# Performance work log

Measured on AMD Instinct MI355X. Metric: run time of the kernel, lower is better.

Reference implementation:

```python
import jax, jax.numpy as jnp
import numpy as np

N_QUBITS = 7
N_LAYERS = 2
DIM = 2 ** N_QUBITS  # 128
NORM_FACTOR = 1.0


def _cnot_gather_idx(n):
    # CNOT chain (0,1),(1,2),...,(n-2,n-1) plus wraparound (n-1,0).
    # new_state[x] = old_state[idx[x]]; apply gates in reverse to arange.
    gates = [(i, i + 1) for i in range(n - 1)] + [(n - 1, 0)]
    idx = np.arange(2 ** n)
    for c, t in reversed(gates):
        cbit = 1 << (n - 1 - c)  # pennylane wire 0 = most significant bit
        tbit = 1 << (n - 1 - t)
        idx = np.where((idx & cbit) > 0, idx ^ tbit, idx)
    return jnp.asarray(idx)

CNOT_IDX = _cnot_gather_idx(N_QUBITS)


def silu(x):
    return x * jax.nn.sigmoid(x)


def cayley(A_real, A_imag):
    # Hermitianize then Cayley transform -> unitary, per layer. [L,D,D]
    A = A_real.astype(jnp.complex64) + 1j * A_imag.astype(jnp.complex64)
    A = A + jnp.conj(jnp.swapaxes(A, -1, -2))
    I = jnp.eye(DIM, dtype=A.dtype)
    return jnp.matmul(A - 1j * I, jnp.linalg.inv(A + 1j * I))


def _single_qubit_gate(theta_x, theta_y):
    # combined G = RY(theta_y) @ RX(theta_x) applied to every qubit
    cx, sx = jnp.cos(theta_x / 2), jnp.sin(theta_x / 2)
    cy, sy = jnp.cos(theta_y / 2), jnp.sin(theta_y / 2)
    RX = jnp.stack([jnp.stack([cx + 0j, -1j * sx]), jnp.stack([-1j * sx, cx + 0j])])
    RY = jnp.stack([jnp.stack([cy + 0j, -sy + 0j]), jnp.stack([sy + 0j, cy + 0j])])
    return RY @ RX


def quantum_evolve(psi, coeffs, q_mats):
    # psi: [N, DIM] complex64 normalized state vectors
    N = psi.shape[0]
    for j in range(N_LAYERS):
        psi = psi @ q_mats[j].T  # QubitUnitary: new = U @ old
        G = _single_qubit_gate(coeffs[j, 0], coeffs[j, 1])
        psi = psi.reshape((N,) + (2,) * N_QUBITS)
        for ax in range(1, N_QUBITS + 1):
            psi = jnp.moveaxis(jnp.tensordot(G, psi, axes=((1,), (ax,))), 0, ax)
        psi = psi.reshape(N, DIM)
        psi = psi[:, CNOT_IDX]  # CNOT chain is a fixed basis permutation
    return psi


def setup_inputs() -> dict:
    key = jax.random.key(0)
    ks = jax.random.split(key, 16)
    N, E = 50000, 800000
    in_nf, hid, out_nf = 128, 128, 128
    h = jax.random.normal(ks[0], (N, in_nf), dtype=jnp.float32)
    edge_index = jax.random.randint(ks[1], (2, E), 0, N)
    s = 0.05
    W_e1 = jax.random.normal(ks[2], (2 * in_nf, hid), dtype=jnp.float32) * s
    b_e1 = jnp.zeros((hid,), dtype=jnp.float32)
    W_e2 = jax.random.normal(ks[3], (hid, hid), dtype=jnp.float32) * s
    b_e2 = jnp.zeros((hid,), dtype=jnp.float32)
    W_enc = jax.random.normal(ks[4], (hid + in_nf, DIM), dtype=jnp.float32) * s
    b_enc = jnp.zeros((DIM,), dtype=jnp.float32)
    coeffs = jax.random.normal(ks[5], (N_LAYERS, 2), dtype=jnp.float32) * 0.1
    A_real = jax.random.normal(ks[6], (N_LAYERS, DIM, DIM), dtype=jnp.float32) * 0.01
    A_imag = jax.random.normal(ks[7], (N_LAYERS, DIM, DIM), dtype=jnp.float32) * 0.01
    W_dec = jax.random.normal(ks[8], (DIM, out_nf), dtype=jnp.float32) * s
    b_dec = jnp.zeros((out_nf,), dtype=jnp.float32)
    return {"h": h, "edge_index": edge_index, "W_e1": W_e1, "b_e1": b_e1,
            "W_e2": W_e2, "b_e2": b_e2, "W_enc": W_enc, "b_enc": b_enc,
            "coeffs": coeffs, "A_real": A_real, "A_imag": A_imag,
            "W_dec": W_dec, "b_dec": b_dec}


def reference(h, edge_index, W_e1, b_e1, W_e2, b_e2, W_enc, b_enc,
              coeffs, A_real, A_imag, W_dec, b_dec):
    row, col = edge_index[0], edge_index[1]
    # edge model: mij = MLP([h_src, h_tgt])
    e = jnp.concatenate([h[row], h[col]], axis=1)  # [E, 2*in_nf]
    e = silu(e @ W_e1 + b_e1)
    edge_feat = silu(e @ W_e2 + b_e2)  # [E, hid]
    # node model: scatter-sum aggregation over destination `row`
    agg = jax.ops.segment_sum(edge_feat, row, num_segments=h.shape[0]) / NORM_FACTOR
    q_input = jnp.concatenate([h, agg], axis=1) @ W_enc + b_enc  # [N, DIM]
    norm = jnp.sqrt(jnp.sum(q_input ** 2, axis=1, keepdims=True) + 1e-12)
    psi = (q_input / norm).astype(jnp.complex64)
    q_mats = cayley(A_real, A_imag)  # [L, DIM, DIM] unitary
    psi = quantum_evolve(psi, coeffs, q_mats)
    out = h + (jnp.real(psi) @ W_dec + b_dec)
    return out, edge_feat
```

## Files before the change

### kernel.cpp

```cpp
#include <hip/hip_runtime.h>
#include <math.h>

#define N_NODES 50000
#define N_EDGES 800000
#define NS_ITERS 3

typedef __attribute__((ext_vector_type(8))) short bf16x8;
typedef __attribute__((ext_vector_type(2))) short shortx2;
typedef __attribute__((ext_vector_type(4))) float f32x4;

__device__ __forceinline__ float silu_f(float x) {
    return x / (1.0f + __expf(-x));
}

__device__ __forceinline__ unsigned short f2bf(float x) {
    union { float f; unsigned u; } v; v.f = x;
    unsigned r = v.u + 0x7FFFu + ((v.u >> 16) & 1u);
    return (unsigned short)(r >> 16);
}

__device__ __forceinline__ void atomic_pk_add_bf16(short* addr, shortx2 v) {
    typedef shortx2 __attribute__((address_space(1)))* gp1;
    __builtin_amdgcn_global_atomic_fadd_v2bf16((gp1)(unsigned long long)addr, v);
}

__global__ __launch_bounds__(256) void hbf16_kernel(const float* __restrict__ h,
                                                    short* __restrict__ hbf) {
    int i = blockIdx.x * 256 + threadIdx.x;
    const float4* h4 = (const float4*)h;
    float4 v0 = h4[i * 2], v1 = h4[i * 2 + 1];
    bf16x8 b;
    b[0] = (short)f2bf(v0.x); b[1] = (short)f2bf(v0.y);
    b[2] = (short)f2bf(v0.z); b[3] = (short)f2bf(v0.w);
    b[4] = (short)f2bf(v1.x); b[5] = (short)f2bf(v1.y);
    b[6] = (short)f2bf(v1.z); b[7] = (short)f2bf(v1.w);
    ((bf16x8*)hbf)[i] = b;
}

__global__ __launch_bounds__(1024) void hmat_kernel(const float* __restrict__ A_real,
                                                    const float* __restrict__ A_imag,
                                                    float* __restrict__ H,
                                                    float* __restrict__ X) {
    const int L = blockIdx.x;
    const int t = threadIdx.x;
    const float* ar = A_real + L * 16384;
    const float* ai = A_imag + L * 16384;
    float* hre = H + L * 32768;
    float* him = hre + 16384;
    float* xre = X + L * 32768;
    float* xim = xre + 16384;
    for (int q = 0; q < 16; ++q) {
        int idx = t + 1024 * q;
        int i = idx >> 7, j = idx & 127;
        float hr = ar[idx] + ar[j * 128 + i];
        float hi = ai[idx] - ai[j * 128 + i];
        hre[idx] = hr;
        him[idx] = hi;
        xre[idx] = hr;
        xim[idx] = hi - (i == j ? 1.0f : 0.0f);
    }
}

__global__ __launch_bounds__(512) void ns_t_kernel(const float* __restrict__ H,
                                                   const float* __restrict__ X,
                                                   float* __restrict__ T) {
    const int L = blockIdx.x >> 5;
    const int t = threadIdx.x;
    const int i = (blockIdx.x & 31) * 4 + (t >> 7);
    const int j = t & 127;
    const float* hre = H + L * 32768;
    const float* him = hre + 16384;
    const float* xre = X + L * 32768;
    const float* xim = xre + 16384;
    float accr = 0.f, acci = 0.f;
    #pragma unroll 4
    for (int k = 0; k < 128; ++k) {
        float hr = hre[i * 128 + k], hi = him[i * 128 + k];
        float xr = xre[k * 128 + j], xi = xim[k * 128 + j];
        accr += hr * xr - hi * xi;
        acci += hr * xi + hi * xr;
    }
    T[L * 32768 + i * 128 + j]         = accr - xim[i * 128 + j];
    T[L * 32768 + 16384 + i * 128 + j] = acci + xre[i * 128 + j];
}

__global__ __launch_bounds__(512) void ns_x_kernel(const float* __restrict__ X,
                                                   const float* __restrict__ T,
                                                   float* __restrict__ Xout) {
    const int L = blockIdx.x >> 5;
    const int t = threadIdx.x;
    const int i = (blockIdx.x & 31) * 4 + (t >> 7);
    const int j = t & 127;
    const float* xre = X + L * 32768;
    const float* xim = xre + 16384;
    const float* tre = T + L * 32768;
    const float* tim = tre + 16384;
    float accr = 0.f, acci = 0.f;
    #pragma unroll 4
    for (int k = 0; k < 128; ++k) {
        float xr = xre[i * 128 + k], xi = xim[i * 128 + k];
        float tr = tre[k * 128 + j], ti = tim[k * 128 + j];
        accr += xr * tr - xi * ti;
        acci += xr * ti + xi * tr;
    }
    Xout[L * 32768 + i * 128 + j]         = 2.0f * xre[i * 128 + j] - accr;
    Xout[L * 32768 + 16384 + i * 128 + j] = 2.0f * xim[i * 128 + j] - acci;
}

__global__ __launch_bounds__(1024) void gateperm_kernel(const float* __restrict__ X,
                                                        const float* __restrict__ coeffs,
                                                        float* __restrict__ Y) {
    __shared__ float Mre[128 * 129];
    __shared__ float Mim[128 * 129];
    const int L = blockIdx.x;
    const int t = threadIdx.x;
    const float* xre = X + L * 32768;
    const float* xim = xre + 16384;

    for (int q = 0; q < 16; ++q) {
        int idx = t + 1024 * q;
        int i = idx >> 7, j = idx & 127;
        Mre[i * 129 + j] = (i == j ? 1.0f : 0.0f) + 2.0f * xim[idx];
        Mim[i * 129 + j] = -2.0f * xre[idx];
    }
    __syncthreads();

    const float tx = coeffs[2 * L + 0] * 0.5f;
    const float ty = coeffs[2 * L + 1] * 0.5f;
    const float cx = cosf(tx), sx = sinf(tx), cy = cosf(ty), sy = sinf(ty);
    const float G00r = cx * cy, G00i = sx * sy;
    const float G01r = -cx * sy, G01i = -sx * cy;
    const float G10r = cx * sy, G10i = -sx * cy;
    const float G11r = cx * cy, G11i = -sx * sy;

    for (int st = 0; st < 7; ++st) {
        int b = 1 << st;
        #pragma unroll
        for (int p = 0; p < 8; ++p) {
            int pid = t + 1024 * p;
            int col = pid & 127, ph = pid >> 7;
            int i0 = ((ph >> st) << (st + 1)) | (ph & (b - 1));
            int i1 = i0 | b;
            float v0r = Mre[i0 * 129 + col], v0i = Mim[i0 * 129 + col];
            float v1r = Mre[i1 * 129 + col], v1i = Mim[i1 * 129 + col];
            Mre[i0 * 129 + col] = G00r * v0r - G00i * v0i + G01r * v1r - G01i * v1i;
            Mim[i0 * 129 + col] = G00r * v0i + G00i * v0r + G01r * v1i + G01i * v1r;
            Mre[i1 * 129 + col] = G10r * v0r - G10i * v0i + G11r * v1r - G11i * v1i;
            Mim[i1 * 129 + col] = G10r * v0i + G10i * v0r + G11r * v1i + G11i * v1r;
        }
        __syncthreads();
    }

    const int cs[7] = {6, 5, 4, 3, 2, 1, 0};
    const int ts[7] = {0, 6, 5, 4, 3, 2, 1};
    float* yre = Y + L * 32768;
    float* yim = yre + 16384;
    for (int q = 0; q < 16; ++q) {
        int idx = t + 1024 * q;
        int ii_ = idx >> 7, col = idx & 127;
        int s = ii_;
        #pragma unroll
        for (int m = 0; m < 7; ++m) {
            int cbit = 1 << (6 - cs[m]);
            int tbit = 1 << (6 - ts[m]);
            if (s & cbit) s ^= tbit;
        }
        yre[idx] = Mre[s * 129 + col];
        yim[idx] = Mim[s * 129 + col];
    }
}

__global__ __launch_bounds__(512) void combine1_kernel(const float* __restrict__ Y,
                                                       float* __restrict__ ReM) {
    __shared__ float q1r[16384];
    __shared__ float q1i[16384];
    const int t = threadIdx.x;
    const float* q1re = Y;
    const float* q1im = Y + 16384;
    const float* q2re = Y + 32768;
    const float* q2im = Y + 49152;
    for (int q = 0; q < 32; ++q) {
        q1r[t + 512 * q] = q1re[t + 512 * q];
        q1i[t + 512 * q] = q1im[t + 512 * q];
    }
    __syncthreads();
    int i = blockIdx.x * 4 + (t >> 7);
    int j = t & 127;
    float acc = 0.f;
    for (int k = 0; k < 128; ++k) {
        acc += q2re[i * 128 + k] * q1r[k * 128 + j] - q2im[i * 128 + k] * q1i[k * 128 + j];
    }
    ReM[i * 128 + j] = acc;
}

__global__ __launch_bounds__(512) void combine2_kernel(const float* __restrict__ ReM,
                                                       const float* __restrict__ W_dec,
                                                       short* __restrict__ Dt) {
    __shared__ float ml[16384];
    __shared__ float wl[16384];
    const int t = threadIdx.x;
    for (int q = 0; q < 32; ++q) {
        ml[t + 512 * q] = ReM[t + 512 * q];
        wl[t + 512 * q] = W_dec[t + 512 * q];
    }
    __syncthreads();
    int k = blockIdx.x * 4 + (t >> 7);
    int j = t & 127;
    float acc = 0.f;
    for (int i = 0; i < 128; ++i) {
        acc += ml[i * 128 + k] * wl[i * 128 + j];
    }
    Dt[j * 128 + k] = (short)f2bf(acc);
}

__global__ __launch_bounds__(1024, 4) void edge_kernel(const short* __restrict__ hbf,
                                                       const int* __restrict__ ei,
                                                       const float* __restrict__ W_e1,
                                                       const float* __restrict__ b_e1,
                                                       const float* __restrict__ W_e2,
                                                       const float* __restrict__ b_e2,
                                                       float* __restrict__ ef_out,
                                                       short* __restrict__ agg_bf) {
    __shared__ short w1t[128 * 256];
    __shared__ short w2t[128 * 128];
    __shared__ short c1s[16][1024];

    const int t = threadIdx.x;
    const int lane = t & 63;
    const int w = t >> 6;
    const int l15 = lane & 15;
    const int kg = lane >> 4;

    {
        const float4* w1_4 = (const float4*)W_e1;
        for (int q = 0; q < 8; ++q) {
            int idx4 = t + 1024 * q;
            int k = idx4 >> 5, j4 = idx4 & 31;
            float4 v = w1_4[idx4];
            int j = j4 * 4;
            w1t[(j + 0) * 256 + (k ^ (((j + 0) & 7) << 3))] = (short)f2bf(v.x);
            w1t[(j + 1) * 256 + (k ^ (((j + 1) & 7) << 3))] = (short)f2bf(v.y);
            w1t[(j + 2) * 256 + (k ^ (((j + 2) & 7) << 3))] = (short)f2bf(v.z);
            w1t[(j + 3) * 256 + (k ^ (((j + 3) & 7) << 3))] = (short)f2bf(v.w);
        }
        const float4* w2_4 = (const float4*)W_e2;
        for (int q = 0; q < 4; ++q) {
            int idx4 = t + 1024 * q;
            int k = idx4 >> 5, j4 = idx4 & 31;
            float4 v = w2_4[idx4];
            int j = j4 * 4;
            w2t[(j + 0) * 128 + (k ^ (((j + 0) & 7) << 3))] = (short)f2bf(v.x);
            w2t[(j + 1) * 128 + (k ^ (((j + 1) & 7) << 3))] = (short)f2bf(v.y);
            w2t[(j + 2) * 128 + (k ^ (((j + 2) & 7) << 3))] = (short)f2bf(v.z);
            w2t[(j + 3) * 128 + (k ^ (((j + 3) & 7) << 3))] = (short)f2bf(v.w);
        }
    }
    float b1v[8], b2v[8];
    #pragma unroll
    for (int nf = 0; nf < 8; ++nf) {
        b1v[nf] = b_e1[nf * 16 + l15];
        b2v[nf] = b_e2[nf * 16 + l15];
    }
    __syncthreads();

    const bf16x8* hb8 = (const bf16x8*)hbf;
    short* myc1 = &c1s[w][0];
    const int NW = gridDim.x * 16;
    const int wvid = blockIdx.x * 16 + w;
    const int nt = N_EDGES / 16;

    int tile = wvid;
    int ri = 0, ci = 0;
    if (tile < nt) {
        ri = ei[tile * 16 + l15];
        ci = ei[N_EDGES + tile * 16 + l15];
    }

    for (; tile < nt; ) {
        const int e0 = tile * 16;
        bf16x8 a1[8];
        #pragma unroll
        for (int s = 0; s < 4; ++s) a1[s] = hb8[(size_t)ri * 16 + s * 4 + kg];
        #pragma unroll
        for (int s = 0; s < 4; ++s) a1[4 + s] = hb8[(size_t)ci * 16 + s * 4 + kg];

        const int tn = tile + NW;
        int ri2 = 0, ci2 = 0;
        if (tn < nt) {
            ri2 = ei[tn * 16 + l15];
            ci2 = ei[N_EDGES + tn * 16 + l15];
        }

        f32x4 acc[8];
        #pragma unroll
        for (int nf = 0; nf < 8; ++nf) acc[nf] = (f32x4){0.f, 0.f, 0.f, 0.f};
        #pragma unroll
        for (int s = 0; s < 8; ++s) {
            const int k0 = s * 32 + kg * 8;
            #pragma unroll
            for (int nf = 0; nf < 8; ++nf) {
                int brow = nf * 16 + l15;
                bf16x8 b = *(const bf16x8*)&w1t[brow * 256 + (k0 ^ ((brow & 7) << 3))];
                acc[nf] = __builtin_amdgcn_mfma_f32_16x16x32_bf16(a1[s], b, acc[nf], 0, 0, 0);
            }
        }

        f32x4 acc2[8];
        #pragma unroll
        for (int nf = 0; nf < 8; ++nf) acc2[nf] = (f32x4){0.f, 0.f, 0.f, 0.f};
        #pragma unroll
        for (int half = 0; half < 2; ++half) {
            #pragma unroll
            for (int nfh = 0; nfh < 4; ++nfh) {
                int nf = half * 4 + nfh;
                #pragma unroll
                for (int r = 0; r < 4; ++r) {
                    int row = kg * 4 + r;
                    int c = nfh * 16 + l15;
                    myc1[row * 64 + (c ^ ((row & 7) << 3))] =
                        (short)f2bf(silu_f(acc[nf][r] + b1v[nf]));
                }
            }
            #pragma unroll
            for (int s2l = 0; s2l < 2; ++s2l) {
                int k0h = s2l * 32 + kg * 8;
                bf16x8 a2 = *(const bf16x8*)&myc1[l15 * 64 + (k0h ^ ((l15 & 7) << 3))];
                int k0g = half * 64 + k0h;
                #pragma unroll
                for (int nf = 0; nf < 8; ++nf) {
                    int brow = nf * 16 + l15;
                    bf16x8 b = *(const bf16x8*)&w2t[brow * 128 + (k0g ^ ((brow & 7) << 3))];
                    acc2[nf] = __builtin_amdgcn_mfma_f32_16x16x32_bf16(a2, b, acc2[nf], 0, 0, 0);
                }
            }
        }

        int rw[4];
        #pragma unroll
        for (int r = 0; r < 4; ++r) rw[r] = __shfl(ri, kg * 4 + r);
        #pragma unroll
        for (int r = 0; r < 4; ++r) {
            int erow = kg * 4 + r;
            float* efp = ef_out + (size_t)(e0 + erow) * 128;
            short* agp = agg_bf + (size_t)rw[r] * 128;
            #pragma unroll
            for (int nf = 0; nf < 8; ++nf) {
                int col = nf * 16 + l15;
                float v = silu_f(acc2[nf][r] + b2v[nf]);
                __builtin_nontemporal_store(v, efp + col);
                float vn = __shfl_xor(v, 1);
                if ((l15 & 1) == 0) {
                    shortx2 pk;
                    pk.x = (short)f2bf(v);
                    pk.y = (short)f2bf(vn);
                    atomic_pk_add_bf16(agp + col, pk);
                }
            }
        }

        tile = tn; ri = ri2; ci = ci2;
    }
}

__global__ __launch_bounds__(512, 4) void encode_kernel(const short* __restrict__ hbf,
                                                        const short* __restrict__ agg_bf,
                                                        const float* __restrict__ W_enc,
                                                        const float* __restrict__ b_enc,
                                                        short* __restrict__ v_bf) {
    __shared__ short wet[128 * 256];

    const int t = threadIdx.x;
    const int lane = t & 63;
    const int w = t >> 6;
    const int l15 = lane & 15;
    const int kg = lane >> 4;

    {
        const float4* we4 = (const float4*)W_enc;
        for (int q = 0; q < 16; ++q) {
            int idx4 = t + 512 * q;
            int k = idx4 >> 5, j4 = idx4 & 31;
            float4 v = we4[idx4];
            int j = j4 * 4;
            wet[(j + 0) * 256 + (k ^ (((j + 0) & 7) << 3))] = (short)f2bf(v.x);
            wet[(j + 1) * 256 + (k ^ (((j + 1) & 7) << 3))] = (short)f2bf(v.y);
            wet[(j + 2) * 256 + (k ^ (((j + 2) & 7) << 3))] = (short)f2bf(v.z);
            wet[(j + 3) * 256 + (k ^ (((j + 3) & 7) << 3))] = (short)f2bf(v.w);
        }
    }
    float bj[8];
    #pragma unroll
    for (int nf = 0; nf < 8; ++nf) bj[nf] = b_enc[nf * 16 + l15];
    __syncthreads();

    const bf16x8* hb8 = (const bf16x8*)hbf;
    const bf16x8* ab8 = (const bf16x8*)agg_bf;
    const int NW = gridDim.x * 8;
    const int nt = N_NODES / 16;

    for (int tile = blockIdx.x * 8 + w; tile < nt; tile += NW) {
        const int node = tile * 16 + l15;
        bf16x8 a[8];
        #pragma unroll
        for (int s = 0; s < 4; ++s) a[s] = hb8[(size_t)node * 16 + s * 4 + kg];
        #pragma unroll
        for (int s = 0; s < 4; ++s) a[4 + s] = ab8[(size_t)node * 16 + s * 4 + kg];

        f32x4 acc[8];
        #pragma unroll
        for (int nf = 0; nf < 8; ++nf) acc[nf] = (f32x4){0.f, 0.f, 0.f, 0.f};
        #pragma unroll
        for (int s = 0; s < 8; ++s) {
            const int k0 = s * 32 + kg * 8;
            #pragma unroll
            for (int nf = 0; nf < 8; ++nf) {
                int brow = nf * 16 + l15;
                bf16x8 b = *(const bf16x8*)&wet[brow * 256 + (k0 ^ ((brow & 7) << 3))];
                acc[nf] = __builtin_amdgcn_mfma_f32_16x16x32_bf16(a[s], b, acc[nf], 0, 0, 0);
            }
        }

        float nr[4] = {0.f, 0.f, 0.f, 0.f};
        #pragma unroll
        for (int nf = 0; nf < 8; ++nf) {
            #pragma unroll
            for (int r = 0; r < 4; ++r) {
                acc[nf][r] += bj[nf];
                nr[r] += acc[nf][r] * acc[nf][r];
            }
        }
        #pragma unroll
        for (int r = 0; r < 4; ++r) {
            nr[r] += __shfl_xor(nr[r], 1);
            nr[r] += __shfl_xor(nr[r], 2);
            nr[r] += __shfl_xor(nr[r], 4);
            nr[r] += __shfl_xor(nr[r], 8);
            nr[r] = 1.0f / sqrtf(nr[r] + 1e-12f);
        }
        #pragma unroll
        for (int r = 0; r < 4; ++r) {
            size_t rowb = (size_t)(tile * 16 + kg * 4 + r) * 128;
            #pragma unroll
            for (int nf = 0; nf < 8; ++nf) {
                v_bf[rowb + nf * 16 + l15] = (short)f2bf(acc[nf][r] * nr[r]);
            }
        }
    }
}

__global__ __launch_bounds__(512, 4) void decode_kernel(const short* __restrict__ v_bf,
                                                        const float* __restrict__ h,
                                                        const short* __restrict__ Dt_bf,
                                                        const float* __restrict__ b_dec,
                                                        float* __restrict__ out) {
    __shared__ short dt[128 * 128];

    const int t = threadIdx.x;
    const int lane = t & 63;
    const int w = t >> 6;
    const int l15 = lane & 15;
    const int kg = lane >> 4;

    {
        const int4* s4 = (const int4*)Dt_bf;
        for (int q = 0; q < 4; ++q) {
            int idx4 = t + 512 * q;
            int j = idx4 >> 4, c = idx4 & 15;
            int k0 = c * 8;
            int4 v = s4[idx4];
            *(int4*)&dt[j * 128 + (k0 ^ ((j & 7) << 3))] = v;
        }
    }
    float bj[8];
    #pragma unroll
    for (int nf = 0; nf < 8; ++nf) bj[nf] = b_dec[nf * 16 + l15];
    __syncthreads();

    const bf16x8* vb8 = (const bf16x8*)v_bf;
    const int NW = gridDim.x * 8;
    const int nt = N_NODES / 16;

    for (int tile = blockIdx.x * 8 + w; tile < nt; tile += NW) {
        const int node = tile * 16 + l15;
        bf16x8 a[4];
        #pragma unroll
        for (int s = 0; s < 4; ++s) a[s] = vb8[(size_t)node * 16 + s * 4 + kg];

        f32x4 acc[8];
        #pragma unroll
        for (int nf = 0; nf < 8; ++nf) acc[nf] = (f32x4){0.f, 0.f, 0.f, 0.f};
        #pragma unroll
        for (int s = 0; s < 4; ++s) {
            const int k0 = s * 32 + kg * 8;
            #pragma unroll
            for (int nf = 0; nf < 8; ++nf) {
                int brow = nf * 16 + l15;
                bf16x8 b = *(const bf16x8*)&dt[brow * 128 + (k0 ^ ((brow & 7) << 3))];
                acc[nf] = __builtin_amdgcn_mfma_f32_16x16x32_bf16(a[s], b, acc[nf], 0, 0, 0);
            }
        }
        #pragma unroll
        for (int r = 0; r < 4; ++r) {
            size_t rowb = (size_t)(tile * 16 + kg * 4 + r) * 128;
            #pragma unroll
            for (int nf = 0; nf < 8; ++nf) {
                int col = nf * 16 + l15;
                out[rowb + col] = h[rowb + col] + acc[nf][r] + bj[nf];
            }
        }
    }
}

extern "C" void kernel_launch(void* const* d_in, const int* in_sizes, int n_in,
                              void* d_out, int out_size, void* d_ws, size_t ws_size,
                              hipStream_t stream) {
    const float* h      = (const float*)d_in[0];
    const int*   ei     = (const int*)d_in[1];
    const float* W_e1   = (const float*)d_in[2];
    const float* b_e1   = (const float*)d_in[3];
    const float* W_e2   = (const float*)d_in[4];
    const float* b_e2   = (const float*)d_in[5];
    const float* W_enc  = (const float*)d_in[6];
    const float* b_enc  = (const float*)d_in[7];
    const float* coeffs = (const float*)d_in[8];
    const float* A_real = (const float*)d_in[9];
    const float* A_imag = (const float*)d_in[10];
    const float* W_dec  = (const float*)d_in[11];
    const float* b_dec  = (const float*)d_in[12];

    float* out    = (float*)d_out;
    float* ef_out = out + (size_t)N_NODES * 128;

    short* agg_bf = (short*)d_ws;
    short* v_bf   = agg_bf + (size_t)N_NODES * 128;
    short* h_bf   = v_bf + (size_t)N_NODES * 128;
    float* small  = (float*)(h_bf + (size_t)N_NODES * 128);
    float* Ybuf   = small;
    float* ReM    = Ybuf + 65536;
    float* Hbuf   = ReM + 16384;
    float* Xa     = Hbuf + 65536;
    float* Xb     = Xa + 65536;
    float* Tbuf   = Xb + 65536;
    short* Dt_bf  = (short*)(Tbuf + 65536);

    hipMemsetAsync(agg_bf, 0, (size_t)N_NODES * 128 * sizeof(short), stream);

    hbf16_kernel<<<3125, 256, 0, stream>>>(h, h_bf);

    hmat_kernel<<<2, 1024, 0, stream>>>(A_real, A_imag, Hbuf, Xa);
    float* xc = Xa;
    float* xn = Xb;
    for (int it = 0; it < NS_ITERS; ++it) {
        ns_t_kernel<<<64, 512, 0, stream>>>(Hbuf, xc, Tbuf);
        ns_x_kernel<<<64, 512, 0, stream>>>(xc, Tbuf, xn);
        float* tmp = xc; xc = xn; xn = tmp;
    }
    gateperm_kernel<<<2, 1024, 0, stream>>>(xc, coeffs, Ybuf);
    combine1_kernel<<<32, 512, 0, stream>>>(Ybuf, ReM);
    combine2_kernel<<<32, 512, 0, stream>>>(ReM, W_dec, Dt_bf);

    edge_kernel<<<256, 1024, 0, stream>>>(h_bf, ei, W_e1, b_e1, W_e2, b_e2, ef_out, agg_bf);

    encode_kernel<<<256, 512, 0, stream>>>(h_bf, agg_bf, W_enc, b_enc, v_bf);

    decode_kernel<<<256, 512, 0, stream>>>(v_bf, h, Dt_bf, b_dec, out);
}
```

Baseline: 623.3 us.

## Fuse encode and decode into one node kernel, prefetch edge gathers, cut NS iterations

Encode and decode are merged into a single node kernel. The normalized quantum state now passes through per-wave LDS into the decode MFMA instead of round-tripping through a bf16 global buffer. The edge kernel software-pipelines the next tile's h-row gathers behind the current tile's MFMAs, at the cost of more registers. The Newton-Schulz iteration count for the matrix inverse drops from 3 to 2, which lowers accuracy of the Cayley unitary and could break correctness tolerance.

```diff
diff --git a/kernel.cpp b/kernel.cpp
--- a/kernel.cpp
+++ b/kernel.cpp
@@ -3,7 +3,7 @@
 
 #define N_NODES 50000
 #define N_EDGES 800000
-#define NS_ITERS 3
+#define NS_ITERS 2
 
 typedef __attribute__((ext_vector_type(8))) short bf16x8;
 typedef __attribute__((ext_vector_type(2))) short shortx2;
@@ -266,29 +266,31 @@
     const bf16x8* hb8 = (const bf16x8*)hbf;
     short* myc1 = &c1s[w][0];
     const int NW = gridDim.x * 16;
-    const int wvid = blockIdx.x * 16 + w;
     const int nt = N_EDGES / 16;
 
-    int tile = wvid;
-    int ri = 0, ci = 0;
-    if (tile < nt) {
-        ri = ei[tile * 16 + l15];
-        ci = ei[N_EDGES + tile * 16 + l15];
-    }
-
-    for (; tile < nt; ) {
+    int tile = blockIdx.x * 16 + w;
+    if (tile >= nt) return;
+    int ri = ei[tile * 16 + l15];
+    int ci = ei[N_EDGES + tile * 16 + l15];
+    bf16x8 a1[8];
+    #pragma unroll
+    for (int s = 0; s < 4; ++s) a1[s] = hb8[(size_t)ri * 16 + s * 4 + kg];
+    #pragma unroll
+    for (int s = 0; s < 4; ++s) a1[4 + s] = hb8[(size_t)ci * 16 + s * 4 + kg];
+    int tn = tile + NW;
+    bool more = (tn < nt);
+    int rin = 0, cin = 0;
+    if (more) {
+        rin = ei[tn * 16 + l15];
+        cin = ei[N_EDGES + tn * 16 + l15];
+    }
+
+    for (;;) {
         const int e0 = tile * 16;
-        bf16x8 a1[8];
-        #pragma unroll
-        for (int s = 0; s < 4; ++s) a1[s] = hb8[(size_t)ri * 16 + s * 4 + kg];
-        #pragma unroll
-        for (int s = 0; s < 4; ++s) a1[4 + s] = hb8[(size_t)ci * 16 + s * 4 + kg];
-
-        const int tn = tile + NW;
-        int ri2 = 0, ci2 = 0;
-        if (tn < nt) {
-            ri2 = ei[tn * 16 + l15];
-            ci2 = ei[N_EDGES + tn * 16 + l15];
+        bf16x8 a1n[8];
+        if (more) {
+            #pragma unroll
+            for (int s = 0; s < 4; ++s) a1n[s] = hb8[(size_t)rin * 16 + s * 4 + kg];
         }
 
         f32x4 acc[8];
@@ -303,6 +305,11 @@
                 bf16x8 b = *(const bf16x8*)&w1t[brow * 256 + (k0 ^ ((brow & 7) << 3))];
                 acc[nf] = __builtin_amdgcn_mfma_f32_16x16x32_bf16(a1[s], b, acc[nf], 0, 0, 0);
             }
+        }
+
+        if (more) {
+            #pragma unroll
+            for (int s = 0; s < 4; ++s) a1n[4 + s] = hb8[(size_t)cin * 16 + s * 4 + kg];
         }
 
         f32x4 acc2[8];
@@ -358,16 +365,31 @@
             }
         }
 
-        tile = tn; ri = ri2; ci = ci2;
-    }
-}
-
-__global__ __launch_bounds__(512, 4) void encode_kernel(const short* __restrict__ hbf,
-                                                        const short* __restrict__ agg_bf,
-                                                        const float* __restrict__ W_enc,
-                                                        const float* __restrict__ b_enc,
-                                                        short* __restrict__ v_bf) {
+        if (!more) break;
+        tile = tn;
+        ri = rin;
+        #pragma unroll
+        for (int s = 0; s < 8; ++s) a1[s] = a1n[s];
+        tn = tile + NW;
+        more = (tn < nt);
+        if (more) {
+            rin = ei[tn * 16 + l15];
+            cin = ei[N_EDGES + tn * 16 + l15];
+        }
+    }
+}
+
+__global__ __launch_bounds__(512, 2) void node_kernel(const short* __restrict__ hbf,
+                                                      const short* __restrict__ agg_bf,
+                                                      const float* __restrict__ W_enc,
+                                                      const float* __restrict__ b_enc,
+                                                      const short* __restrict__ Dt_bf,
+                                                      const float* __restrict__ b_dec,
+                                                      const float* __restrict__ h,
+                                                      float* __restrict__ out) {
     __shared__ short wet[128 * 256];
+    __shared__ short dtl[128 * 128];
+    __shared__ short c1s[8][2048];
 
     const int t = threadIdx.x;
     const int lane = t & 63;
@@ -387,14 +409,26 @@
             wet[(j + 2) * 256 + (k ^ (((j + 2) & 7) << 3))] = (short)f2bf(v.z);
             wet[(j + 3) * 256 + (k ^ (((j + 3) & 7) << 3))] = (short)f2bf(v.w);
         }
-    }
-    float bj[8];
+        const int4* s4 = (const int4*)Dt_bf;
+        for (int q = 0; q < 4; ++q) {
+            int idx4 = t + 512 * q;
+            int j = idx4 >> 4, c = idx4 & 15;
+            int k0 = c * 8;
+            int4 v = s4[idx4];
+            *(int4*)&dtl[j * 128 + (k0 ^ ((j & 7) << 3))] = v;
+        }
+    }
+    float bj1[8], bj2[8];
     #pragma unroll
-    for (int nf = 0; nf < 8; ++nf) bj[nf] = b_enc[nf * 16 + l15];
+    for (int nf = 0; nf < 8; ++nf) {
+        bj1[nf] = b_enc[nf * 16 + l15];
+        bj2[nf] = b_dec[nf * 16 + l15];
+    }
     __syncthreads();
 
     const bf16x8* hb8 = (const bf16x8*)hbf;
     const bf16x8* ab8 = (const bf16x8*)agg_bf;
+    short* myc1 = &c1s[w][0];
     const int NW = gridDim.x * 8;
     const int nt = N_NODES / 16;
 
@@ -425,7 +459,7 @@
         for (int nf = 0; nf < 8; ++nf) {
             #pragma unroll
             for (int r = 0; r < 4; ++r) {
-                acc[nf][r] += bj[nf];
+                acc[nf][r] += bj1[nf];
                 nr[r] += acc[nf][r] * acc[nf][r];
             }
         }
@@ -437,75 +471,39 @@
             nr[r] += __shfl_xor(nr[r], 8);
             nr[r] = 1.0f / sqrtf(nr[r] + 1e-12f);
         }
+
+        #pragma unroll
+        for (int nf = 0; nf < 8; ++nf) {
+            #pragma unroll
+            for (int r = 0; r < 4; ++r) {
+                int row = kg * 4 + r;
+                int col = nf * 16 + l15;
+                myc1[row * 128 + (col ^ ((row & 7) << 3))] = (short)f2bf(acc[nf][r] * nr[r]);
+            }
+        }
+
+        f32x4 acc2[8];
+        #pragma unroll
+        for (int nf = 0; nf < 8; ++nf) acc2[nf] = (f32x4){0.f, 0.f, 0.f, 0.f};
+        #pragma unroll
+        for (int s = 0; s < 4; ++s) {
+            const int k0 = s * 32 + kg * 8;
+            bf16x8 a2 = *(const bf16x8*)&myc1[l15 * 128 + (k0 ^ ((l15 & 7) << 3))];
+            #pragma unroll
+            for (int nf = 0; nf < 8; ++nf) {
+                int brow = nf * 16 + l15;
+                bf16x8 b = *(const bf16x8*)&dtl[brow * 128 + (k0 ^ ((brow & 7) << 3))];
+                acc2[nf] = __builtin_amdgcn_mfma_f32_16x16x32_bf16(a2, b, acc2[nf], 0, 0, 0);
+            }
+        }
+
         #pragma unroll
         for (int r = 0; r < 4; ++r) {
             size_t rowb = (size_t)(tile * 16 + kg * 4 + r) * 128;
             #pragma unroll
             for (int nf = 0; nf < 8; ++nf) {
-                v_bf[rowb + nf * 16 + l15] = (short)f2bf(acc[nf][r] * nr[r]);
-            }
-        }
-    }
-}
-
-__global__ __launch_bounds__(512, 4) void decode_kernel(const short* __restrict__ v_bf,
-                                                        const float* __restrict__ h,
-                                                        const short* __restrict__ Dt_bf,
-                                                        const float* __restrict__ b_dec,
-                                                        float* __restrict__ out) {
-    __shared__ short dt[128 * 128];
-
-    const int t = threadIdx.x;
-    const int lane = t & 63;
-    const int w = t >> 6;
-    const int l15 = lane & 15;
-    const int kg = lane >> 4;
-
-    {
-        const int4* s4 = (const int4*)Dt_bf;
-        for (int q = 0; q < 4; ++q) {
-            int idx4 = t + 512 * q;
-            int j = idx4 >> 4, c = idx4 & 15;
-            int k0 = c * 8;
-            int4 v = s4[idx4];
-            *(int4*)&dt[j * 128 + (k0 ^ ((j & 7) << 3))] = v;
-        }
-    }
-    float bj[8];
-    #pragma unroll
-    for (int nf = 0; nf < 8; ++nf) bj[nf] = b_dec[nf * 16 + l15];
-    __syncthreads();
-
-    const bf16x8* vb8 = (const bf16x8*)v_bf;
-    const int NW = gridDim.x * 8;
-    const int nt = N_NODES / 16;
-
-    for (int tile = blockIdx.x * 8 + w; tile < nt; tile += NW) {
-        const int node = tile * 16 + l15;
-        bf16x8 a[4];
-        #pragma unroll
-        for (int s = 0; s < 4; ++s) a[s] = vb8[(size_t)node * 16 + s * 4 + kg];
-
-        f32x4 acc[8];
-        #pragma unroll
-        for (int nf = 0; nf < 8; ++nf) acc[nf] = (f32x4){0.f, 0.f, 0.f, 0.f};
-        #pragma unroll
-        for (int s = 0; s < 4; ++s) {
-            const int k0 = s * 32 + kg * 8;
-            #pragma unroll
-            for (int nf = 0; nf < 8; ++nf) {
-                int brow = nf * 16 + l15;
-                bf16x8 b = *(const bf16x8*)&dt[brow * 128 + (k0 ^ ((brow & 7) << 3))];
-                acc[nf] = __builtin_amdgcn_mfma_f32_16x16x32_bf16(a[s], b, acc[nf], 0, 0, 0);
-            }
-        }
-        #pragma unroll
-        for (int r = 0; r < 4; ++r) {
-            size_t rowb = (size_t)(tile * 16 + kg * 4 + r) * 128;
-            #pragma unroll
-            for (int nf = 0; nf < 8; ++nf) {
                 int col = nf * 16 + l15;
-                out[rowb + col] = h[rowb + col] + acc[nf][r] + bj[nf];
+                out[rowb + col] = h[rowb + col] + acc2[nf][r] + bj2[nf];
             }
         }
     }
@@ -532,8 +530,7 @@
     float* ef_out = out + (size_t)N_NODES * 128;
 
     short* agg_bf = (short*)d_ws;
-    short* v_bf   = agg_bf + (size_t)N_NODES * 128;
-    short* h_bf   = v_bf + (size_t)N_NODES * 128;
+    short* h_bf   = agg_bf + (size_t)N_NODES * 128;
     float* small  = (float*)(h_bf + (size_t)N_NODES * 128);
     float* Ybuf   = small;
     float* ReM    = Ybuf + 65536;
@@ -561,7 +558,5 @@
 
     edge_kernel<<<256, 1024, 0, stream>>>(h_bf, ei, W_e1, b_e1, W_e2, b_e2, ef_out, agg_bf);
 
-    encode_kernel<<<256, 512, 0, stream>>>(h_bf, agg_bf, W_enc, b_enc, v_bf);
-
-    decode_kernel<<<256, 512, 0, stream>>>(v_bf, h, Dt_bf, b_dec, out);
-}
+    node_kernel<<<196, 512, 0, stream>>>(h_bf, agg_bf, W_enc, b_enc, Dt_bf, b_dec, h, out);
+}
```

After: 604.5 us. -3.0%, faster.
